# Performance work log

Measured on AMD Instinct MI355X. Metric: run time of the kernel, lower is better.

## Reference

```python
import jax, jax.numpy as jnp
import numpy as np

H = 64  # hidden_size

def _lstm_layer(x_tbf, W_ih, W_hh, b_ih, b_hh):
    # x_tbf: [T, B, F]; W_ih: [4H, F]; W_hh: [4H, H]; biases: [4H]
    T, B, _ = x_tbf.shape
    # precompute input projections for all timesteps at once: [T, B, 4H]
    x_proj = jnp.einsum('tbf,gf->tbg', x_tbf, W_ih) + (b_ih + b_hh)

    def step(carry, xp):
        h, c = carry
        gates = xp + h @ W_hh.T  # [B, 4H]
        i, f, g, o = jnp.split(gates, 4, axis=-1)
        i = jax.nn.sigmoid(i)
        f = jax.nn.sigmoid(f)
        g = jnp.tanh(g)
        o = jax.nn.sigmoid(o)
        c = f * c + i * g
        h = o * jnp.tanh(c)
        return (h, c), h

    h0 = jnp.zeros((B, H), dtype=x_tbf.dtype)
    c0 = jnp.zeros((B, H), dtype=x_tbf.dtype)
    (_, _), hs = jax.lax.scan(step, (h0, c0), x_proj)
    return hs  # [T, B, H]


def setup_inputs() -> dict:
    key = jax.random.key(0)
    ks = jax.random.split(key, 12)
    B, T, F = 1024, 512, 32
    s_in = 1.0 / np.sqrt(H)  # torch LSTM init scale
    u = lambda k, shape: jax.random.uniform(k, shape, jnp.float32, -s_in, s_in)
    return {
        'x': jax.random.normal(ks[0], (B, T, F), jnp.float32),
        'W_ih0': u(ks[1], (4 * H, F)),
        'W_hh0': u(ks[2], (4 * H, H)),
        'b_ih0': u(ks[3], (4 * H,)),
        'b_hh0': u(ks[4], (4 * H,)),
        'W_ih1': u(ks[5], (4 * H, H)),
        'W_hh1': u(ks[6], (4 * H, H)),
        'b_ih1': u(ks[7], (4 * H,)),
        'b_hh1': u(ks[8], (4 * H,)),
        'fc_w': u(ks[9], (1, H)),
        'fc_b': u(ks[10], (1,)),
    }


def reference(x, W_ih0, W_hh0, b_ih0, b_hh0, W_ih1, W_hh1, b_ih1, b_hh1, fc_w, fc_b):
    # x: [B, T, F] (batch_first); run 2 stacked LSTM layers, take last step, linear head
    x_tbf = jnp.transpose(x, (1, 0, 2))  # [T, B, F]
    h1 = _lstm_layer(x_tbf, W_ih0, W_hh0, b_ih0, b_hh0)  # [T, B, H]
    h2 = _lstm_layer(h1, W_ih1, W_hh1, b_ih1, b_hh1)      # [T, B, H]
    last = h2[-1]                                          # [B, H]
    return last @ fc_w.T + fc_b                            # [B, 1]
```

## Files before the change

### kernel.cpp

```cpp
#include <hip/hip_runtime.h>
#include <math.h>

#define H  64
#define F  32
#define NB 4
#define NT 512
#define HS 80

typedef __attribute__((ext_vector_type(8))) short   s8v;
typedef __attribute__((ext_vector_type(8))) __bf16  bf8v;
typedef __attribute__((ext_vector_type(4))) float   f4v;

__device__ __forceinline__ unsigned short f2bf(float x) {
    unsigned u = __builtin_bit_cast(unsigned, x);
    u += 0x7FFFu + ((u >> 16) & 1u);
    return (unsigned short)(u >> 16);
}
__device__ __forceinline__ unsigned cvtpk(float a, float b) {
    unsigned r;
    asm("v_cvt_pk_bf16_f32 %0, %1, %2" : "=v"(r) : "v"(a), "v"(b));
    return r;
}
__device__ __forceinline__ f4v mfma_(s8v a, s8v b, f4v c) {
    return __builtin_amdgcn_mfma_f32_16x16x32_bf16(
        __builtin_bit_cast(bf8v, a), __builtin_bit_cast(bf8v, b), c, 0, 0, 0);
}
__device__ __forceinline__ float sig_(float x) {
    return __builtin_amdgcn_rcpf(1.0f + __expf(-x));
}
__device__ __forceinline__ float tanh_(float x) {
    return 1.0f - 2.0f * __builtin_amdgcn_rcpf(1.0f + __expf(2.0f * x));
}
__device__ __forceinline__ void bar_lds() {
    asm volatile("s_waitcnt lgkmcnt(0)" ::: "memory");
    __builtin_amdgcn_s_barrier();
}

__device__ __forceinline__ s8v load_hi(const float* __restrict__ Wrow, int koff) {
    s8v hi;
    #pragma unroll
    for (int i = 0; i < 8; ++i) hi[i] = (short)f2bf(Wrow[koff + i]);
    return hi;
}

__global__ __launch_bounds__(NT, 2)
void lstm_v9(const float* __restrict__ x,
             const float* __restrict__ Wih0,
             const float* __restrict__ Whh0,
             const float* __restrict__ bih0,
             const float* __restrict__ bhh0,
             const float* __restrict__ Wih1,
             const float* __restrict__ Whh1,
             const float* __restrict__ bih1,
             const float* __restrict__ bhh1,
             const float* __restrict__ fcw,
             const float* __restrict__ fcb,
             float* __restrict__ out,
             int T, int B)
{
    const int tid  = threadIdx.x;
    const int w    = tid >> 6;
    const int wl   = w & 3;
    const bool isL0 = (w < 4);
    const int lane = tid & 63;
    const int j    = lane & 15;
    const int hi4  = lane >> 4;
    const int bm   = j >> 2;
    const int u    = 16 * wl + j;
    const int b0   = blockIdx.x * NB;

    __shared__ alignas(16) unsigned short h0[2][NB][HS];
    __shared__ alignas(16) unsigned short h1[2][NB][HS];
    __shared__ float part[4][64];

    for (int i = tid; i < 2 * NB * HS; i += NT) {
        (&h0[0][0][0])[i] = 0;
        (&h1[0][0][0])[i] = 0;
    }

    if (isL0) {
        s8v wxh[4];
        s8v whh[4][2];
        float bias[4];
        #pragma unroll
        for (int g = 0; g < 4; ++g) {
            const int R = 64 * g + 16 * wl + j;
            wxh[g] = load_hi(&Wih0[R * F], 8 * hi4);
            #pragma unroll
            for (int kt = 0; kt < 2; ++kt)
                whh[g][kt] = load_hi(&Whh0[R * H], 32 * kt + 8 * hi4);
            bias[g] = bih0[R] + bhh0[R];
        }
        const float* xrow = x + ((size_t)(b0 + bm) * T) * F + 8 * hi4;
        float4 xA0 = *(const float4*)(xrow);
        float4 xA1 = *(const float4*)(xrow + 4);
        float4 xB0 = *(const float4*)(xrow + F);
        float4 xB1 = *(const float4*)(xrow + F + 4);

        __syncthreads();

        float c = 0.f;
        auto stepL0 = [&](int s, int par, float4& xr0, float4& xr1) {
            s8v xf;
            unsigned* xfu = (unsigned*)&xf;
            xfu[0] = cvtpk(xr0.x, xr0.y);
            xfu[1] = cvtpk(xr0.z, xr0.w);
            xfu[2] = cvtpk(xr1.x, xr1.y);
            xfu[3] = cvtpk(xr1.z, xr1.w);
            const size_t tld = (size_t)((s + 2 < T) ? (s + 2) : (T - 1)) * F;
            xr0 = *(const float4*)(xrow + tld);
            xr1 = *(const float4*)(xrow + tld + 4);

            const s8v hf0 = *(const s8v*)&h0[par ^ 1][bm][8 * hi4];
            const s8v hf1 = *(const s8v*)&h0[par ^ 1][bm][8 * (4 + hi4)];

            f4v a[4], b[4];
            __builtin_amdgcn_s_setprio(1);
            #pragma unroll
            for (int g = 0; g < 4; ++g) {
                f4v av = {bias[g], bias[g], bias[g], bias[g]};
                a[g] = mfma_(xf, wxh[g], av);
                f4v bv = {0.f, 0.f, 0.f, 0.f};
                bv = mfma_(hf0, whh[g][0], bv);
                b[g] = mfma_(hf1, whh[g][1], bv);
            }
            __builtin_amdgcn_s_setprio(0);
            const float gi = sig_(a[0][0] + b[0][0]);
            const float gf = sig_(a[1][0] + b[1][0]);
            const float gg = tanh_(a[2][0] + b[2][0]);
            const float go = sig_(a[3][0] + b[3][0]);
            c = gf * c + gi * gg;
            const float hv = go * tanh_(c);
            h0[par][hi4][u] = (unsigned short)cvtpk(hv, hv);
            bar_lds();
        };

        #pragma unroll 1
        for (int s = 0; s < T; s += 2) {
            stepL0(s,     0, xA0, xA1);
            stepL0(s + 1, 1, xB0, xB1);
        }
        bar_lds();
    } else {
        s8v wgh[4][2];
        s8v whh[4][2];
        float bias[4];
        #pragma unroll
        for (int g = 0; g < 4; ++g) {
            const int R = 64 * g + 16 * wl + j;
            #pragma unroll
            for (int kt = 0; kt < 2; ++kt) {
                wgh[g][kt] = load_hi(&Wih1[R * H], 32 * kt + 8 * hi4);
                whh[g][kt] = load_hi(&Whh1[R * H], 32 * kt + 8 * hi4);
            }
            bias[g] = bih1[R] + bhh1[R];
        }
        const float fcwr = fcw[u];
        __syncthreads();

        float c = 0.f;
        auto stepL1 = [&](int s, int par) {
            if (s >= 1) {
                const s8v gf0 = *(const s8v*)&h0[par ^ 1][bm][8 * hi4];
                const s8v gf1 = *(const s8v*)&h0[par ^ 1][bm][8 * (4 + hi4)];
                const s8v hf0 = *(const s8v*)&h1[par][bm][8 * hi4];
                const s8v hf1 = *(const s8v*)&h1[par][bm][8 * (4 + hi4)];

                f4v a[4], b[4];
                __builtin_amdgcn_s_setprio(1);
                #pragma unroll
                for (int g = 0; g < 4; ++g) {
                    f4v av = {bias[g], bias[g], bias[g], bias[g]};
                    av = mfma_(gf0, wgh[g][0], av);
                    a[g] = mfma_(gf1, wgh[g][1], av);
                    f4v bv = {0.f, 0.f, 0.f, 0.f};
                    bv = mfma_(hf0, whh[g][0], bv);
                    b[g] = mfma_(hf1, whh[g][1], bv);
                }
                __builtin_amdgcn_s_setprio(0);
                const float gi = sig_(a[0][0] + b[0][0]);
                const float gf = sig_(a[1][0] + b[1][0]);
                const float gg = tanh_(a[2][0] + b[2][0]);
                const float go = sig_(a[3][0] + b[3][0]);
                c = gf * c + gi * gg;
                const float hv = go * tanh_(c);
                if (s < T) {
                    h1[par ^ 1][hi4][u] = (unsigned short)cvtpk(hv, hv);
                } else {
                    part[wl][lane] = hv * fcwr;
                }
            }
            bar_lds();
        };

        #pragma unroll 1
        for (int s = 0; s < T; s += 2) {
            stepL1(s,     0);
            stepL1(s + 1, 1);
        }
        stepL1(T, 0);
    }

    __syncthreads();

    if (tid < 64) {
        float v = part[0][lane] + part[1][lane] + part[2][lane] + part[3][lane];
        v += __shfl_xor(v, 1);
        v += __shfl_xor(v, 2);
        v += __shfl_xor(v, 4);
        v += __shfl_xor(v, 8);
        if (j == 0) out[b0 + hi4] = v + fcb[0];
    }
}

extern "C" void kernel_launch(void* const* d_in, const int* in_sizes, int n_in,
                              void* d_out, int out_size, void* d_ws, size_t ws_size,
                              hipStream_t stream) {
    const float* x    = (const float*)d_in[0];
    const float* Wih0 = (const float*)d_in[1];
    const float* Whh0 = (const float*)d_in[2];
    const float* bih0 = (const float*)d_in[3];
    const float* bhh0 = (const float*)d_in[4];
    const float* Wih1 = (const float*)d_in[5];
    const float* Whh1 = (const float*)d_in[6];
    const float* bih1 = (const float*)d_in[7];
    const float* bhh1 = (const float*)d_in[8];
    const float* fcw  = (const float*)d_in[9];
    const float* fcb  = (const float*)d_in[10];
    float* out = (float*)d_out;

    const int B = out_size;
    const int T = in_sizes[0] / (B * F);

    dim3 grid(B / NB), block(NT);
    hipLaunchKernelGGL(lstm_v9, grid, block, 0, stream,
                       x, Wih0, Whh0, bih0, bhh0,
                       Wih1, Whh1, bih1, bhh1, fcw, fcb,
                       out, T, B);
}
```

Measured before the change: 210.4 us.

## Split each layer's gate rows across twice as many waves with shuffle exchange

```diff
diff --git a/kernel.cpp b/kernel.cpp
--- a/kernel.cpp
+++ b/kernel.cpp
@@ -4,7 +4,7 @@
 #define H  64
 #define F  32
 #define NB 4
-#define NT 512
+#define NT 1024
 #define HS 80
 
 typedef __attribute__((ext_vector_type(8))) short   s8v;
@@ -35,63 +35,73 @@
     asm volatile("s_waitcnt lgkmcnt(0)" ::: "memory");
     __builtin_amdgcn_s_barrier();
 }
-
 __device__ __forceinline__ s8v load_hi(const float* __restrict__ Wrow, int koff) {
     s8v hi;
     #pragma unroll
     for (int i = 0; i < 8; ++i) hi[i] = (short)f2bf(Wrow[koff + i]);
     return hi;
 }
-
-__global__ __launch_bounds__(NT, 2)
-void lstm_v9(const float* __restrict__ x,
-             const float* __restrict__ Wih0,
-             const float* __restrict__ Whh0,
-             const float* __restrict__ bih0,
-             const float* __restrict__ bhh0,
-             const float* __restrict__ Wih1,
-             const float* __restrict__ Whh1,
-             const float* __restrict__ bih1,
-             const float* __restrict__ bhh1,
-             const float* __restrict__ fcw,
-             const float* __restrict__ fcb,
-             float* __restrict__ out,
-             int T, int B)
+__device__ __forceinline__ s8v xfrag(const float4& a, const float4& b) {
+    s8v r; unsigned* ru = (unsigned*)&r;
+    ru[0] = cvtpk(a.x, a.y); ru[1] = cvtpk(a.z, a.w);
+    ru[2] = cvtpk(b.x, b.y); ru[3] = cvtpk(b.z, b.w);
+    return r;
+}
+
+__global__ __launch_bounds__(NT, 4)
+void lstm_v12(const float* __restrict__ x,
+              const float* __restrict__ Wih0,
+              const float* __restrict__ Whh0,
+              const float* __restrict__ bih0,
+              const float* __restrict__ bhh0,
+              const float* __restrict__ Wih1,
+              const float* __restrict__ Whh1,
+              const float* __restrict__ bih1,
+              const float* __restrict__ bhh1,
+              const float* __restrict__ fcw,
+              const float* __restrict__ fcb,
+              float* __restrict__ out,
+              int T, int B)
 {
     const int tid  = threadIdx.x;
     const int w    = tid >> 6;
-    const int wl   = w & 3;
-    const bool isL0 = (w < 4);
+    const bool isL0 = (w < 8);
+    const int wu   = isL0 ? w : (w - 8);
     const int lane = tid & 63;
     const int j    = lane & 15;
     const int hi4  = lane >> 4;
     const int bm   = j >> 2;
-    const int u    = 16 * wl + j;
+    const int q    = j & 7;
+    const int half = j >> 3;
+    const int u    = 8 * wu + q;
+    const int RA   = 64 * half + u;
+    const int RB   = 64 * (2 + half) + u;
     const int b0   = blockIdx.x * NB;
 
     __shared__ alignas(16) unsigned short h0[2][NB][HS];
     __shared__ alignas(16) unsigned short h1[2][NB][HS];
-    __shared__ float part[4][64];
+    __shared__ float part[8][4][8];
 
     for (int i = tid; i < 2 * NB * HS; i += NT) {
         (&h0[0][0][0])[i] = 0;
         (&h1[0][0][0])[i] = 0;
     }
 
+    float c = 0.f;
+
     if (isL0) {
-        s8v wxh[4];
-        s8v whh[4][2];
-        float bias[4];
-        #pragma unroll
-        for (int g = 0; g < 4; ++g) {
-            const int R = 64 * g + 16 * wl + j;
-            wxh[g] = load_hi(&Wih0[R * F], 8 * hi4);
-            #pragma unroll
-            for (int kt = 0; kt < 2; ++kt)
-                whh[g][kt] = load_hi(&Whh0[R * H], 32 * kt + 8 * hi4);
-            bias[g] = bih0[R] + bhh0[R];
-        }
+        s8v wxA, wxB, whA0, whA1, whB0, whB1;
+        wxA  = load_hi(&Wih0[RA * F], 8 * hi4);
+        wxB  = load_hi(&Wih0[RB * F], 8 * hi4);
+        whA0 = load_hi(&Whh0[RA * H], 8 * hi4);
+        whA1 = load_hi(&Whh0[RA * H], 32 + 8 * hi4);
+        whB0 = load_hi(&Whh0[RB * H], 8 * hi4);
+        whB1 = load_hi(&Whh0[RB * H], 32 + 8 * hi4);
+        const float biasA = bih0[RA] + bhh0[RA];
+        const float biasB = bih0[RB] + bhh0[RB];
+
         const float* xrow = x + ((size_t)(b0 + bm) * T) * F + 8 * hi4;
+        const int tmax = T - 1;
         float4 xA0 = *(const float4*)(xrow);
         float4 xA1 = *(const float4*)(xrow + 4);
         float4 xB0 = *(const float4*)(xrow + F);
@@ -99,39 +109,43 @@
 
         __syncthreads();
 
-        float c = 0.f;
-        auto stepL0 = [&](int s, int par, float4& xr0, float4& xr1) {
-            s8v xf;
-            unsigned* xfu = (unsigned*)&xf;
-            xfu[0] = cvtpk(xr0.x, xr0.y);
-            xfu[1] = cvtpk(xr0.z, xr0.w);
-            xfu[2] = cvtpk(xr1.x, xr1.y);
-            xfu[3] = cvtpk(xr1.z, xr1.w);
-            const size_t tld = (size_t)((s + 2 < T) ? (s + 2) : (T - 1)) * F;
-            xr0 = *(const float4*)(xrow + tld);
-            xr1 = *(const float4*)(xrow + tld + 4);
+        auto stepL0 = [&](int s, int par, float4& r0, float4& r1) {
+            const s8v xf = xfrag(r0, r1);
+            const size_t tld = (size_t)((s + 2 < tmax) ? (s + 2) : tmax) * F;
+            r0 = *(const float4*)(xrow + tld);
+            r1 = *(const float4*)(xrow + tld + 4);
 
             const s8v hf0 = *(const s8v*)&h0[par ^ 1][bm][8 * hi4];
             const s8v hf1 = *(const s8v*)&h0[par ^ 1][bm][8 * (4 + hi4)];
 
-            f4v a[4], b[4];
             __builtin_amdgcn_s_setprio(1);
-            #pragma unroll
-            for (int g = 0; g < 4; ++g) {
-                f4v av = {bias[g], bias[g], bias[g], bias[g]};
-                a[g] = mfma_(xf, wxh[g], av);
-                f4v bv = {0.f, 0.f, 0.f, 0.f};
-                bv = mfma_(hf0, whh[g][0], bv);
-                b[g] = mfma_(hf1, whh[g][1], bv);
-            }
+            f4v aA = {biasA, biasA, biasA, biasA};
+            aA = mfma_(xf, wxA, aA);
+            f4v bA = {0.f, 0.f, 0.f, 0.f};
+            bA = mfma_(hf0, whA0, bA);
+            bA = mfma_(hf1, whA1, bA);
+            f4v aB = {biasB, biasB, biasB, biasB};
+            aB = mfma_(xf, wxB, aB);
+            f4v bB = {0.f, 0.f, 0.f, 0.f};
+            bB = mfma_(hf0, whB0, bB);
+            bB = mfma_(hf1, whB1, bB);
             __builtin_amdgcn_s_setprio(0);
-            const float gi = sig_(a[0][0] + b[0][0]);
-            const float gf = sig_(a[1][0] + b[1][0]);
-            const float gg = tanh_(a[2][0] + b[2][0]);
-            const float go = sig_(a[3][0] + b[3][0]);
+
+            const float vA = aA[0] + bA[0];
+            const float vB = aB[0] + bB[0];
+            const float pA = __shfl_xor(vA, 8);
+            const float pB = __shfl_xor(vB, 8);
+            const float iv = half ? pA : vA;
+            const float fv = half ? vA : pA;
+            const float gv = half ? pB : vB;
+            const float ov = half ? vB : pB;
+            const float gi = sig_(iv);
+            const float gf = sig_(fv);
+            const float gg = tanh_(gv);
+            const float go = sig_(ov);
             c = gf * c + gi * gg;
             const float hv = go * tanh_(c);
-            h0[par][hi4][u] = (unsigned short)cvtpk(hv, hv);
+            if (half == 0) h0[par][hi4][u] = (unsigned short)cvtpk(hv, hv);
             bar_lds();
         };
 
@@ -142,23 +156,21 @@
         }
         bar_lds();
     } else {
-        s8v wgh[4][2];
-        s8v whh[4][2];
-        float bias[4];
-        #pragma unroll
-        for (int g = 0; g < 4; ++g) {
-            const int R = 64 * g + 16 * wl + j;
-            #pragma unroll
-            for (int kt = 0; kt < 2; ++kt) {
-                wgh[g][kt] = load_hi(&Wih1[R * H], 32 * kt + 8 * hi4);
-                whh[g][kt] = load_hi(&Whh1[R * H], 32 * kt + 8 * hi4);
-            }
-            bias[g] = bih1[R] + bhh1[R];
-        }
-        const float fcwr = fcw[u];
+        s8v wgA0, wgA1, wgB0, wgB1, whA0, whA1, whB0, whB1;
+        wgA0 = load_hi(&Wih1[RA * H], 8 * hi4);
+        wgA1 = load_hi(&Wih1[RA * H], 32 + 8 * hi4);
+        wgB0 = load_hi(&Wih1[RB * H], 8 * hi4);
+        wgB1 = load_hi(&Wih1[RB * H], 32 + 8 * hi4);
+        whA0 = load_hi(&Whh1[RA * H], 8 * hi4);
+        whA1 = load_hi(&Whh1[RA * H], 32 + 8 * hi4);
+        whB0 = load_hi(&Whh1[RB * H], 8 * hi4);
+        whB1 = load_hi(&Whh1[RB * H], 32 + 8 * hi4);
+        const float biasA = bih1[RA] + bhh1[RA];
+        const float biasB = bih1[RB] + bhh1[RB];
+        const float fcwr  = fcw[u];
+
         __syncthreads();
 
-        float c = 0.f;
         auto stepL1 = [&](int s, int par) {
             if (s >= 1) {
                 const s8v gf0 = *(const s8v*)&h0[par ^ 1][bm][8 * hi4];
@@ -166,28 +178,39 @@
                 const s8v hf0 = *(const s8v*)&h1[par][bm][8 * hi4];
                 const s8v hf1 = *(const s8v*)&h1[par][bm][8 * (4 + hi4)];
 
-                f4v a[4], b[4];
                 __builtin_amdgcn_s_setprio(1);
-                #pragma unroll
-                for (int g = 0; g < 4; ++g) {
-                    f4v av = {bias[g], bias[g], bias[g], bias[g]};
-                    av = mfma_(gf0, wgh[g][0], av);
-                    a[g] = mfma_(gf1, wgh[g][1], av);
-                    f4v bv = {0.f, 0.f, 0.f, 0.f};
-                    bv = mfma_(hf0, whh[g][0], bv);
-                    b[g] = mfma_(hf1, whh[g][1], bv);
-                }
+                f4v aA = {biasA, biasA, biasA, biasA};
+                aA = mfma_(gf0, wgA0, aA);
+                aA = mfma_(gf1, wgA1, aA);
+                f4v bA = {0.f, 0.f, 0.f, 0.f};
+                bA = mfma_(hf0, whA0, bA);
+                bA = mfma_(hf1, whA1, bA);
+                f4v aB = {biasB, biasB, biasB, biasB};
+                aB = mfma_(gf0, wgB0, aB);
+                aB = mfma_(gf1, wgB1, aB);
+                f4v bB = {0.f, 0.f, 0.f, 0.f};
+                bB = mfma_(hf0, whB0, bB);
+                bB = mfma_(hf1, whB1, bB);
                 __builtin_amdgcn_s_setprio(0);
-                const float gi = sig_(a[0][0] + b[0][0]);
-                const float gf = sig_(a[1][0] + b[1][0]);
-                const float gg = tanh_(a[2][0] + b[2][0]);
-                const float go = sig_(a[3][0] + b[3][0]);
+
+                const float vA = aA[0] + bA[0];
+                const float vB = aB[0] + bB[0];
+                const float pA = __shfl_xor(vA, 8);
+                const float pB = __shfl_xor(vB, 8);
+                const float iv = half ? pA : vA;
+                const float fv = half ? vA : pA;
+                const float gv = half ? pB : vB;
+                const float ov = half ? vB : pB;
+                const float gi = sig_(iv);
+                const float gf = sig_(fv);
+                const float gg = tanh_(gv);
+                const float go = sig_(ov);
                 c = gf * c + gi * gg;
                 const float hv = go * tanh_(c);
                 if (s < T) {
-                    h1[par ^ 1][hi4][u] = (unsigned short)cvtpk(hv, hv);
+                    if (half == 0) h1[par ^ 1][hi4][u] = (unsigned short)cvtpk(hv, hv);
                 } else {
-                    part[wl][lane] = hv * fcwr;
+                    if (half == 0) part[wu][hi4][q] = hv * fcwr;
                 }
             }
             bar_lds();
@@ -204,12 +227,17 @@
     __syncthreads();
 
     if (tid < 64) {
-        float v = part[0][lane] + part[1][lane] + part[2][lane] + part[3][lane];
+        const int b = tid >> 4, r = tid & 15;
+        float v = 0.f;
+        if (r < 8) {
+            #pragma unroll
+            for (int ww = 0; ww < 8; ++ww) v += part[ww][b][r];
+        }
         v += __shfl_xor(v, 1);
         v += __shfl_xor(v, 2);
         v += __shfl_xor(v, 4);
         v += __shfl_xor(v, 8);
-        if (j == 0) out[b0 + hi4] = v + fcb[0];
+        if (r == 0) out[b0 + b] = v + fcb[0];
     }
 }
 
@@ -233,7 +261,7 @@
     const int T = in_sizes[0] / (B * F);
 
     dim3 grid(B / NB), block(NT);
-    hipLaunchKernelGGL(lstm_v9, grid, block, 0, stream,
+    hipLaunchKernelGGL(lstm_v12, grid, block, 0, stream,
                        x, Wih0, Whh0, bih0, bhh0,
                        Wih1, Whh1, bih1, bhh1, fcw, fcb,
                        out, T, B);
```

Result: slower. 290.1 us (+37.9%).

## Split LSTM step into MFMA and activation phases with two barriers per step

Applied to the files above, without the earlier changes.

```diff
diff --git a/kernel.cpp b/kernel.cpp
--- a/kernel.cpp
+++ b/kernel.cpp
@@ -35,28 +35,33 @@
     asm volatile("s_waitcnt lgkmcnt(0)" ::: "memory");
     __builtin_amdgcn_s_barrier();
 }
-
 __device__ __forceinline__ s8v load_hi(const float* __restrict__ Wrow, int koff) {
     s8v hi;
     #pragma unroll
     for (int i = 0; i < 8; ++i) hi[i] = (short)f2bf(Wrow[koff + i]);
     return hi;
 }
+__device__ __forceinline__ s8v xfrag(const float4& a, const float4& b) {
+    s8v r; unsigned* ru = (unsigned*)&r;
+    ru[0] = cvtpk(a.x, a.y); ru[1] = cvtpk(a.z, a.w);
+    ru[2] = cvtpk(b.x, b.y); ru[3] = cvtpk(b.z, b.w);
+    return r;
+}
 
 __global__ __launch_bounds__(NT, 2)
-void lstm_v9(const float* __restrict__ x,
-             const float* __restrict__ Wih0,
-             const float* __restrict__ Whh0,
-             const float* __restrict__ bih0,
-             const float* __restrict__ bhh0,
-             const float* __restrict__ Wih1,
-             const float* __restrict__ Whh1,
-             const float* __restrict__ bih1,
-             const float* __restrict__ bhh1,
-             const float* __restrict__ fcw,
-             const float* __restrict__ fcb,
-             float* __restrict__ out,
-             int T, int B)
+void lstm_v13(const float* __restrict__ x,
+              const float* __restrict__ Wih0,
+              const float* __restrict__ Whh0,
+              const float* __restrict__ bih0,
+              const float* __restrict__ bhh0,
+              const float* __restrict__ Wih1,
+              const float* __restrict__ Whh1,
+              const float* __restrict__ bih1,
+              const float* __restrict__ bhh1,
+              const float* __restrict__ fcw,
+              const float* __restrict__ fcb,
+              float* __restrict__ out,
+              int T, int B)
 {
     const int tid  = threadIdx.x;
     const int w    = tid >> 6;
@@ -86,61 +91,64 @@
         for (int g = 0; g < 4; ++g) {
             const int R = 64 * g + 16 * wl + j;
             wxh[g] = load_hi(&Wih0[R * F], 8 * hi4);
-            #pragma unroll
-            for (int kt = 0; kt < 2; ++kt)
-                whh[g][kt] = load_hi(&Whh0[R * H], 32 * kt + 8 * hi4);
+            whh[g][0] = load_hi(&Whh0[R * H], 8 * hi4);
+            whh[g][1] = load_hi(&Whh0[R * H], 32 + 8 * hi4);
             bias[g] = bih0[R] + bhh0[R];
         }
         const float* xrow = x + ((size_t)(b0 + bm) * T) * F + 8 * hi4;
-        float4 xA0 = *(const float4*)(xrow);
-        float4 xA1 = *(const float4*)(xrow + 4);
-        float4 xB0 = *(const float4*)(xrow + F);
-        float4 xB1 = *(const float4*)(xrow + F + 4);
+        const int tmax = T - 1;
+        float4 p0 = *(const float4*)(xrow);
+        float4 p1 = *(const float4*)(xrow + 4);
+        s8v xf = xfrag(p0, p1);
+        const size_t o1 = (size_t)((1 < tmax) ? 1 : tmax) * F;
+        const size_t o2 = (size_t)((2 < tmax) ? 2 : tmax) * F;
+        float4 xB0 = *(const float4*)(xrow + o1), xB1 = *(const float4*)(xrow + o1 + 4);
+        float4 xA0 = *(const float4*)(xrow + o2), xA1 = *(const float4*)(xrow + o2 + 4);
 
         __syncthreads();
 
         float c = 0.f;
-        auto stepL0 = [&](int s, int par, float4& xr0, float4& xr1) {
-            s8v xf;
-            unsigned* xfu = (unsigned*)&xf;
-            xfu[0] = cvtpk(xr0.x, xr0.y);
-            xfu[1] = cvtpk(xr0.z, xr0.w);
-            xfu[2] = cvtpk(xr1.x, xr1.y);
-            xfu[3] = cvtpk(xr1.z, xr1.w);
-            const size_t tld = (size_t)((s + 2 < T) ? (s + 2) : (T - 1)) * F;
-            xr0 = *(const float4*)(xrow + tld);
-            xr1 = *(const float4*)(xrow + tld + 4);
-
-            const s8v hf0 = *(const s8v*)&h0[par ^ 1][bm][8 * hi4];
-            const s8v hf1 = *(const s8v*)&h0[par ^ 1][bm][8 * (4 + hi4)];
-
-            f4v a[4], b[4];
-            __builtin_amdgcn_s_setprio(1);
-            #pragma unroll
-            for (int g = 0; g < 4; ++g) {
-                f4v av = {bias[g], bias[g], bias[g], bias[g]};
-                a[g] = mfma_(xf, wxh[g], av);
-                f4v bv = {0.f, 0.f, 0.f, 0.f};
-                bv = mfma_(hf0, whh[g][0], bv);
-                b[g] = mfma_(hf1, whh[g][1], bv);
-            }
-            __builtin_amdgcn_s_setprio(0);
-            const float gi = sig_(a[0][0] + b[0][0]);
-            const float gf = sig_(a[1][0] + b[1][0]);
-            const float gg = tanh_(a[2][0] + b[2][0]);
-            const float go = sig_(a[3][0] + b[3][0]);
-            c = gf * c + gi * gg;
-            const float hv = go * tanh_(c);
-            h0[par][hi4][u] = (unsigned short)cvtpk(hv, hv);
+        f4v accA[4], accB[4];
+
+        auto phA = [&](int s, int par) {
+            if (s < T) {
+                const s8v hf0 = *(const s8v*)&h0[par ^ 1][bm][8 * hi4];
+                const s8v hf1 = *(const s8v*)&h0[par ^ 1][bm][8 * (4 + hi4)];
+                __builtin_amdgcn_s_setprio(1);
+                #pragma unroll
+                for (int g = 0; g < 4; ++g) {
+                    f4v av = {bias[g], bias[g], bias[g], bias[g]};
+                    accA[g] = mfma_(xf, wxh[g], av);
+                    f4v bv = {0.f, 0.f, 0.f, 0.f};
+                    bv = mfma_(hf0, whh[g][0], bv);
+                    accB[g] = mfma_(hf1, whh[g][1], bv);
+                }
+                __builtin_amdgcn_s_setprio(0);
+            }
             bar_lds();
         };
+        auto phB = [&](int s, int par, float4& n0, float4& n1) {
+            if (s < T) {
+                const float gi = sig_(accA[0][0] + accB[0][0]);
+                const float gf = sig_(accA[1][0] + accB[1][0]);
+                const float gg = tanh_(accA[2][0] + accB[2][0]);
+                const float go = sig_(accA[3][0] + accB[3][0]);
+                c = gf * c + gi * gg;
+                const float hv = go * tanh_(c);
+                h0[par][hi4][u] = (unsigned short)cvtpk(hv, hv);
+                xf = xfrag(n0, n1);
+                const size_t tld = (size_t)((s + 3 < tmax) ? (s + 3) : tmax) * F;
+                n0 = *(const float4*)(xrow + tld);
+                n1 = *(const float4*)(xrow + tld + 4);
+            }
+            bar_lds();
+        };
 
         #pragma unroll 1
-        for (int s = 0; s < T; s += 2) {
-            stepL0(s,     0, xA0, xA1);
-            stepL0(s + 1, 1, xB0, xB1);
-        }
-        bar_lds();
+        for (int s = 0; s < T + 2; s += 2) {
+            phA(s, 0);     phB(s, 0, xB0, xB1);
+            phA(s + 1, 1); phB(s + 1, 1, xA0, xA1);
+        }
     } else {
         s8v wgh[4][2];
         s8v whh[4][2];
@@ -148,57 +156,57 @@
         #pragma unroll
         for (int g = 0; g < 4; ++g) {
             const int R = 64 * g + 16 * wl + j;
-            #pragma unroll
-            for (int kt = 0; kt < 2; ++kt) {
-                wgh[g][kt] = load_hi(&Wih1[R * H], 32 * kt + 8 * hi4);
-                whh[g][kt] = load_hi(&Whh1[R * H], 32 * kt + 8 * hi4);
-            }
+            wgh[g][0] = load_hi(&Wih1[R * H], 8 * hi4);
+            wgh[g][1] = load_hi(&Wih1[R * H], 32 + 8 * hi4);
+            whh[g][0] = load_hi(&Whh1[R * H], 8 * hi4);
+            whh[g][1] = load_hi(&Whh1[R * H], 32 + 8 * hi4);
             bias[g] = bih1[R] + bhh1[R];
         }
         const float fcwr = fcw[u];
         __syncthreads();
 
         float c = 0.f;
-        auto stepL1 = [&](int s, int par) {
-            if (s >= 1) {
-                const s8v gf0 = *(const s8v*)&h0[par ^ 1][bm][8 * hi4];
-                const s8v gf1 = *(const s8v*)&h0[par ^ 1][bm][8 * (4 + hi4)];
+        f4v accA[4], accB[4];
+
+        #pragma unroll 1
+        for (int s = 0; s <= T + 1; ++s) {
+            const int par = s & 1;
+            s8v gf0 = {}, gf1 = {};
+            if (s >= 1 && s <= T) {
+                gf0 = *(const s8v*)&h0[par ^ 1][bm][8 * hi4];
+                gf1 = *(const s8v*)&h0[par ^ 1][bm][8 * (4 + hi4)];
+            }
+            if (s >= 2) {
+                const float gi = sig_(accA[0][0] + accB[0][0]);
+                const float gf = sig_(accA[1][0] + accB[1][0]);
+                const float gg = tanh_(accA[2][0] + accB[2][0]);
+                const float go = sig_(accA[3][0] + accB[3][0]);
+                c = gf * c + gi * gg;
+                const float hv = go * tanh_(c);
+                if (s <= T) {
+                    h1[par][hi4][u] = (unsigned short)cvtpk(hv, hv);
+                } else {
+                    part[wl][lane] = hv * fcwr;
+                }
+            }
+            bar_lds();
+            if (s >= 1 && s <= T) {
                 const s8v hf0 = *(const s8v*)&h1[par][bm][8 * hi4];
                 const s8v hf1 = *(const s8v*)&h1[par][bm][8 * (4 + hi4)];
-
-                f4v a[4], b[4];
                 __builtin_amdgcn_s_setprio(1);
                 #pragma unroll
                 for (int g = 0; g < 4; ++g) {
                     f4v av = {bias[g], bias[g], bias[g], bias[g]};
                     av = mfma_(gf0, wgh[g][0], av);
-                    a[g] = mfma_(gf1, wgh[g][1], av);
+                    accA[g] = mfma_(gf1, wgh[g][1], av);
                     f4v bv = {0.f, 0.f, 0.f, 0.f};
                     bv = mfma_(hf0, whh[g][0], bv);
-                    b[g] = mfma_(hf1, whh[g][1], bv);
+                    accB[g] = mfma_(hf1, whh[g][1], bv);
                 }
                 __builtin_amdgcn_s_setprio(0);
-                const float gi = sig_(a[0][0] + b[0][0]);
-                const float gf = sig_(a[1][0] + b[1][0]);
-                const float gg = tanh_(a[2][0] + b[2][0]);
-                const float go = sig_(a[3][0] + b[3][0]);
-                c = gf * c + gi * gg;
-                const float hv = go * tanh_(c);
-                if (s < T) {
-                    h1[par ^ 1][hi4][u] = (unsigned short)cvtpk(hv, hv);
-                } else {
-                    part[wl][lane] = hv * fcwr;
-                }
-            }
-            bar_lds();
-        };
-
-        #pragma unroll 1
-        for (int s = 0; s < T; s += 2) {
-            stepL1(s,     0);
-            stepL1(s + 1, 1);
-        }
-        stepL1(T, 0);
+            }
+            bar_lds();
+        }
     }
 
     __syncthreads();
@@ -233,7 +241,7 @@
     const int T = in_sizes[0] / (B * F);
 
     dim3 grid(B / NB), block(NT);
-    hipLaunchKernelGGL(lstm_v9, grid, block, 0, stream,
+    hipLaunchKernelGGL(lstm_v13, grid, block, 0, stream,
                        x, Wih0, Whh0, bih0, bhh0,
                        Wih1, Whh1, bih1, bhh1, fcw, fcb,
                        out, T, B);
```

Measured after the change: 248.8 us. 18.3% more time.
